# Performance work log

Hardware: AMD Instinct MI355X
Metric: run time of the kernel (lower is better)

## Reference

```python
import jax, jax.numpy as jnp
import numpy as np

B, H, S, D = 65536, 1024, 1024, 128  # batch, hidden_dim, memory_slots, slot_size
WRITE_THRESHOLD = 0.01


def setup_inputs() -> dict:
    key = jax.random.key(0)
    ks = jax.random.split(key, 6)
    return {
        "query": jax.random.normal(ks[0], (B, H), jnp.float32),
        "content": jax.random.normal(ks[1], (B, H), jnp.float32),
        "memory": jax.random.normal(ks[2], (S, D), jnp.float32),
        "memory_age": jnp.zeros((S,), jnp.float32),
        "W_read": jax.random.normal(ks[3], (H, S), jnp.float32) * 0.02,
        "b_read": jnp.zeros((S,), jnp.float32),
        "W_write": jax.random.normal(ks[4], (H, S), jnp.float32) * 0.02,
        "b_write": jnp.zeros((S,), jnp.float32),
        "W_content": jax.random.normal(ks[5], (H, D), jnp.float32) * 0.02,
        "b_content": jnp.zeros((D,), jnp.float32),
    }


def reference(query, content, memory, memory_age, W_read, b_read,
              W_write, b_write, W_content, b_content):
    # ---- read: attention-based addressing over memory slots ----
    read_weights = jax.nn.softmax(query @ W_read + b_read, axis=-1)   # [B, S]
    read_content = read_weights @ memory                              # [B, D]

    # ---- write: vectorized consolidation update (replaces per-slot python loop) ----
    write_weights = jax.nn.softmax(query @ W_write + b_write, axis=-1)  # [B, S]
    w_mean = write_weights.mean(axis=0)                                 # [S]
    c_mean = (content @ W_content + b_content).mean(axis=0)             # [D]
    mask = w_mean > WRITE_THRESHOLD                                     # [S] bool
    consolidation = jax.nn.sigmoid(memory_age * 0.1)                    # [S]
    f = (w_mean * consolidation)[:, None]                               # [S, 1]
    updated = (1.0 - f) * memory + f * c_mean[None, :]                  # [S, D]
    new_memory = jnp.where(mask[:, None], updated, memory)
    new_memory_age = memory_age + mask.astype(memory_age.dtype)

    return read_content, new_memory, new_memory_age
```

## Files before the change

### kernel.cpp

```cpp
#include <hip/hip_runtime.h>
#include <hip/hip_fp16.h>
#include <cstdint>
#include <cstddef>

#define B_N 65536
#define H_N 1024
#define S_N 1024
#define D_N 128

typedef __attribute__((ext_vector_type(8))) short bf16x8;
typedef __attribute__((ext_vector_type(8))) _Float16 f16x8;
typedef __attribute__((ext_vector_type(4))) float f32x4;

#define MFMA_BF(a, b, c) __builtin_amdgcn_mfma_f32_16x16x32_bf16((a), (b), (c), 0, 0, 0)
#define MFMA_F16(a, b, c) __builtin_amdgcn_mfma_f32_16x16x32_f16((a), (b), (c), 0, 0, 0)

__device__ __forceinline__ unsigned short f2bf(float f) {
    unsigned u = __float_as_uint(f);
    u += 0x7FFFu + ((u >> 16) & 1u);
    return (unsigned short)(u >> 16);
}
__device__ __forceinline__ float h2f(unsigned short h) {
    return __half2float(__ushort_as_half(h));
}
__device__ __forceinline__ unsigned short f2h(float f) {
    return __half_as_ushort(__float2half_rn(f));
}
__device__ __forceinline__ void async16(void* lds, const void* g) {
    __builtin_amdgcn_global_load_lds(
        (const __attribute__((address_space(1))) unsigned int*)g,
        (__attribute__((address_space(3))) unsigned int*)lds, 16, 0, 0);
}

__global__ void k_zero(float* p, int n) {
    int i = blockIdx.x * blockDim.x + threadIdx.x;
    if (i < n) p[i] = 0.f;
}

__global__ __launch_bounds__(256) void k_prep_q(const float* __restrict__ q,
                                                unsigned short* __restrict__ qb) {
    size_t i = ((size_t)blockIdx.x * 256 + threadIdx.x) * 8;
    float4 a = *(const float4*)(q + i);
    float4 b = *(const float4*)(q + i + 4);
    uint4 o;
    o.x = (unsigned)f2bf(a.x) | ((unsigned)f2bf(a.y) << 16);
    o.y = (unsigned)f2bf(a.z) | ((unsigned)f2bf(a.w) << 16);
    o.z = (unsigned)f2bf(b.x) | ((unsigned)f2bf(b.y) << 16);
    o.w = (unsigned)f2bf(b.z) | ((unsigned)f2bf(b.w) << 16);
    *(uint4*)(qb + i) = o;
}

__global__ __launch_bounds__(256) void k_prep_w(const float* __restrict__ Wr,
                                                const float* __restrict__ Ww,
                                                unsigned short* __restrict__ wcat) {
    __shared__ float t[32][33];
    const int kb = blockIdx.x * 32, nb = blockIdx.y * 32;
    const float* src = blockIdx.z ? Ww : Wr;
    const int tx = threadIdx.x & 31, ty = threadIdx.x >> 5;
#pragma unroll
    for (int i = 0; i < 4; i++) {
        int r = ty + i * 8;
        t[r][tx] = src[(size_t)(kb + r) * S_N + nb + tx];
    }
    __syncthreads();
    unsigned short* dst = wcat + (size_t)blockIdx.z * 1024 * 1024;
#pragma unroll
    for (int i = 0; i < 4; i++) {
        int r = ty + i * 8;
        dst[(size_t)(nb + r) * 1024 + kb + tx] = f2bf(t[tx][r]);
    }
}

__global__ __launch_bounds__(256) void k_prep_mem(const float* __restrict__ mem,
                                                  unsigned short* __restrict__ memT) {
    __shared__ float t[32][33];
    const int db = blockIdx.x * 32, sb = blockIdx.y * 32;
    const int tx = threadIdx.x & 31, ty = threadIdx.x >> 5;
#pragma unroll
    for (int i = 0; i < 4; i++) {
        int r = ty + i * 8;
        t[r][tx] = mem[(size_t)(sb + r) * D_N + db + tx];
    }
    __syncthreads();
#pragma unroll
    for (int i = 0; i < 4; i++) {
        int r = ty + i * 8;
        memT[(size_t)(db + r) * 1024 + sb + tx] = f2h(t[tx][r]);
    }
}

__global__ __launch_bounds__(256) void k_content(const float* __restrict__ content,
                                                 float* __restrict__ csum) {
    const int tid = threadIdx.x;
    const size_t r0 = (size_t)blockIdx.x * 128;
    float4 a = {0.f, 0.f, 0.f, 0.f};
    const float* base = content + r0 * H_N + tid * 4;
#pragma unroll 8
    for (int r = 0; r < 128; r++) {
        float4 v = *(const float4*)(base + (size_t)r * H_N);
        a.x += v.x; a.y += v.y; a.z += v.z; a.w += v.w;
    }
    atomicAdd(&csum[tid * 4 + 0], a.x);
    atomicAdd(&csum[tid * 4 + 1], a.y);
    atomicAdd(&csum[tid * 4 + 2], a.z);
    atomicAdd(&csum[tid * 4 + 3], a.w);
}

#define BARX() asm volatile("s_barrier" ::: "memory")
#define LGK0() asm volatile("s_waitcnt lgkmcnt(0)" ::: "memory")
#define VMC4() asm volatile("s_waitcnt vmcnt(4)" ::: "memory")

__device__ __forceinline__ bf16x8 ldfrag(const char* buf, int row, int ko) {
    int off = (row * 128 + ko) ^ ((row & 7) << 4);
    return *(const bf16x8*)(buf + off);
}
__device__ __forceinline__ void rd_a(const char* bufA, int wm, int l16, int g, int mh,
                                     bf16x8 a[4][2]) {
#pragma unroll
    for (int m2 = 0; m2 < 4; m2++) {
        int row = wm * 128 + (mh * 4 + m2) * 16 + l16;
#pragma unroll
        for (int ks = 0; ks < 2; ks++) a[m2][ks] = ldfrag(bufA, row, ks * 64 + g * 16);
    }
}
__device__ __forceinline__ void rd_b(const char* bufB, int wn, int l16, int g, int nh,
                                     bf16x8 b[2][2]) {
#pragma unroll
    for (int n2 = 0; n2 < 2; n2++) {
        int row = wn * 64 + (nh * 2 + n2) * 16 + l16;
#pragma unroll
        for (int ks = 0; ks < 2; ks++) b[n2][ks] = ldfrag(bufB, row, ks * 64 + g * 16);
    }
}
__device__ __forceinline__ void mm16(f32x4 acc[8][4], bf16x8 a[4][2], bf16x8 b[2][2],
                                     int mh, int nh) {
    __builtin_amdgcn_s_setprio(1);
#pragma unroll
    for (int m2 = 0; m2 < 4; m2++)
#pragma unroll
        for (int n2 = 0; n2 < 2; n2++) {
            f32x4 c = acc[mh * 4 + m2][nh * 2 + n2];
            c = MFMA_BF(a[m2][0], b[n2][0], c);
            c = MFMA_BF(a[m2][1], b[n2][1], c);
            acc[mh * 4 + m2][nh * 2 + n2] = c;
        }
    __builtin_amdgcn_s_setprio(0);
}

__global__ __launch_bounds__(512, 2) void k_gemm(const unsigned short* __restrict__ qb,
                                                 const unsigned short* __restrict__ wcat,
                                                 const float* __restrict__ b_read,
                                                 const float* __restrict__ b_write,
                                                 unsigned short* __restrict__ logits) {
    __shared__ __align__(16) char sm[131072];
    const int tid = threadIdx.x;
    const int w = tid >> 6, lane = tid & 63;
    const int wm = w >> 2, wn = w & 3;
    const int l16 = lane & 15, g = lane >> 4;

    const int nwg = (int)gridDim.y * 8;
    const int lin = (int)blockIdx.y * 8 + (int)blockIdx.x;
    const int nlin = (lin & 7) * (nwg >> 3) + (lin >> 3);
    const int by = nlin >> 3, bx = nlin & 7;
    const size_t mrow = (size_t)by * 256;

    int g0[2];
#pragma unroll
    for (int j = 0; j < 2; j++) {
        int c = w * 64 + j * 512 + lane;
        int lc = (c * 16) ^ (((c >> 3) & 7) << 4);
        g0[j] = (lc >> 7) * 2048 + (lc & 127);
    }
    const char* aB = (const char*)qb + mrow * 2048;
    const char* wB = (const char*)wcat + (size_t)bx * 256 * 2048;
    char* smW = (char*)sm + w * 1024;

#define STG(d, opb, h, ktB) do {                                              \
        const char* s_ = ((opb) ? wB : aB) + ((h) * 262144 + (ktB));          \
        char* d_ = smW + ((d) * 65536 + (opb) * 32768 + (h) * 16384);         \
        async16(d_,        s_ + g0[0]);                                       \
        async16(d_ + 8192, s_ + g0[1]);                                       \
    } while (0)

    f32x4 acc[8][4];
#pragma unroll
    for (int m = 0; m < 8; m++)
#pragma unroll
        for (int n = 0; n < 4; n++) acc[m][n] = (f32x4){0.f, 0.f, 0.f, 0.f};

    const char* bufA0 = (const char*)sm;
    const char* bufB0 = (const char*)sm + 32768;
    const char* bufA1 = (const char*)sm + 65536;
    const char* bufB1 = (const char*)sm + 98304;
    bf16x8 a[4][2], b0[2][2], b1[2][2];

    STG(0, 0, 0, 0); STG(0, 1, 0, 0); STG(0, 0, 1, 0); STG(0, 1, 1, 0);
    STG(1, 1, 0, 128); STG(1, 1, 1, 128);
    VMC4(); BARX();

#pragma unroll 1
    for (int i = 0; i < 8; i++) {
        const int kA = (2 * i + 1) * 128;
        int t2 = 2 * i + 2; if (t2 > 15) t2 = 15;
        int t3 = 2 * i + 3; if (t3 > 15) t3 = 15;
        const int kB = t2 * 128, kC = t3 * 128;

        rd_a(bufA0, wm, l16, g, 0, a); rd_b(bufB0, wn, l16, g, 0, b0);
        STG(1, 0, 0, kA);
        BARX(); LGK0(); mm16(acc, a, b0, 0, 0); BARX();
        rd_b(bufB0, wn, l16, g, 1, b1);
        STG(1, 0, 1, kA);
        BARX(); LGK0(); mm16(acc, a, b1, 0, 1); BARX();
        rd_a(bufA0, wm, l16, g, 1, a);
        STG(0, 1, 0, kB);
        BARX(); LGK0(); mm16(acc, a, b1, 1, 1); BARX();
        STG(0, 1, 1, kB);
        VMC4(); BARX(); mm16(acc, a, b0, 1, 0); BARX();

        rd_a(bufA1, wm, l16, g, 0, a); rd_b(bufB1, wn, l16, g, 0, b0);
        STG(0, 0, 0, kB);
        BARX(); LGK0(); mm16(acc, a, b0, 0, 0); BARX();
        rd_b(bufB1, wn, l16, g, 1, b1);
        STG(0, 0, 1, kB);
        BARX(); LGK0(); mm16(acc, a, b1, 0, 1); BARX();
        rd_a(bufA1, wm, l16, g, 1, a);
        STG(1, 1, 0, kC);
        BARX(); LGK0(); mm16(acc, a, b1, 1, 1); BARX();
        STG(1, 1, 1, kC);
        VMC4(); BARX(); mm16(acc, a, b0, 1, 0); BARX();
    }
#undef STG

    const float* bias = (bx < 4) ? (b_read + bx * 256) : (b_write + bx * 256 - 1024);
#pragma unroll
    for (int nt = 0; nt < 4; nt++) {
        const int col = wn * 64 + nt * 16 + l16;
        const float bv = bias[col];
#pragma unroll
        for (int mt = 0; mt < 8; mt++) {
            const int row0 = wm * 128 + mt * 16 + g * 4;
#pragma unroll
            for (int r = 0; r < 4; r++) {
                float e = __expf(acc[mt][nt][r] + bv);
                logits[(mrow + row0 + r) * 2048 + (size_t)bx * 256 + col] = f2h(e);
            }
        }
    }
}

__global__ __launch_bounds__(256) void k_post(const unsigned short* __restrict__ logits,
                                              const unsigned short* __restrict__ memT,
                                              float* __restrict__ out,
                                              float* __restrict__ wpart, int blk0) {
    __shared__ unsigned short L[16 * 2056];
    __shared__ float sInvR[16], sInvW[16];
    const int tid = threadIdx.x;
    const size_t r0 = (size_t)blockIdx.x * 16;
#pragma unroll
    for (int i = 0; i < 16; i++) {
        int c2 = i * 256 + tid;
        int r = c2 >> 8, off = (c2 & 255) * 8;
        *(uint4*)&L[r * 2056 + off] = *(const uint4*)&logits[(r0 + r) * 2048 + off];
    }
    __syncthreads();
    {
        const int r = tid >> 4, sub = tid & 15;
        const unsigned* row = (const unsigned*)&L[r * 2056];
        float zr = 0.f, zw = 0.f;
#pragma unroll 8
        for (int i = 0; i < 32; i++) {
            unsigned u = row[i * 16 + sub];
            zr += h2f((unsigned short)(u & 0xffff)) + h2f((unsigned short)(u >> 16));
            unsigned v = row[512 + i * 16 + sub];
            zw += h2f((unsigned short)(v & 0xffff)) + h2f((unsigned short)(v >> 16));
        }
        zr += __shfl_xor(zr, 1); zr += __shfl_xor(zr, 2);
        zr += __shfl_xor(zr, 4); zr += __shfl_xor(zr, 8);
        zw += __shfl_xor(zw, 1); zw += __shfl_xor(zw, 2);
        zw += __shfl_xor(zw, 4); zw += __shfl_xor(zw, 8);
        if (sub == 0) { sInvR[r] = 1.f / zr; sInvW[r] = 1.f / zw; }
    }
    __syncthreads();
    const int wave = tid >> 6, lane = tid & 63;
    const int l16 = lane & 15, g = lane >> 4;
    f32x4 acc0 = (f32x4){0.f, 0.f, 0.f, 0.f}, acc1 = acc0;
    for (int k0 = 0; k0 < 1024; k0 += 32) {
        f16x8 a  = *(const f16x8*)&L[l16 * 2056 + k0 + g * 8];
        f16x8 b0 = *(const f16x8*)&memT[(size_t)(wave * 32 + l16) * 1024 + k0 + g * 8];
        f16x8 b1 = *(const f16x8*)&memT[(size_t)(wave * 32 + 16 + l16) * 1024 + k0 + g * 8];
        acc0 = MFMA_F16(a, b0, acc0);
        acc1 = MFMA_F16(a, b1, acc1);
    }
#pragma unroll
    for (int r = 0; r < 4; r++) {
        int row = g * 4 + r;
        float iz = sInvR[row];
        out[(r0 + row) * D_N + wave * 32 + l16] = acc0[r] * iz;
        out[(r0 + row) * D_N + wave * 32 + 16 + l16] = acc1[r] * iz;
    }
    float c0 = 0.f, c1 = 0.f, c2 = 0.f, c3 = 0.f;
#pragma unroll
    for (int r = 0; r < 16; r++) {
        float iz = sInvW[r];
        uint2 u = *(const uint2*)&L[r * 2056 + 1024 + tid * 4];
        c0 += h2f((unsigned short)(u.x & 0xffff)) * iz;
        c1 += h2f((unsigned short)(u.x >> 16)) * iz;
        c2 += h2f((unsigned short)(u.y & 0xffff)) * iz;
        c3 += h2f((unsigned short)(u.y >> 16)) * iz;
    }
    float4 o = {c0, c1, c2, c3};
    *(float4*)&wpart[(size_t)(blk0 + blockIdx.x) * 1024 + tid * 4] = o;
}

__global__ __launch_bounds__(256) void k_wreduce(const float* __restrict__ wpart,
                                                 float* __restrict__ wsum) {
    const int c = (blockIdx.x & 3) * 256 + threadIdx.x;
    const int i0 = (blockIdx.x >> 2) * 512;
    float s0 = 0.f, s1 = 0.f;
    for (int i = 0; i < 512; i += 2) {
        s0 += wpart[(size_t)(i0 + i) * 1024 + c];
        s1 += wpart[(size_t)(i0 + i + 1) * 1024 + c];
    }
    atomicAdd(&wsum[c], s0 + s1);
}

__global__ void k_cmean(const float* __restrict__ csum, const float* __restrict__ Wc,
                        const float* __restrict__ bc, float* __restrict__ cmean) {
    const int d = blockIdx.x, t = threadIdx.x;
    float s = 0.f;
#pragma unroll
    for (int j = 0; j < 16; j++) {
        int h = j * 64 + t;
        s += csum[h] * Wc[h * D_N + d];
    }
#pragma unroll
    for (int o = 1; o < 64; o <<= 1) s += __shfl_xor(s, o);
    if (t == 0) cmean[d] = s * (1.0f / (float)B_N) + bc[d];
}

__global__ __launch_bounds__(256) void k_final(const float* __restrict__ memory,
                                               const float* __restrict__ age,
                                               const float* __restrict__ wsum,
                                               const float* __restrict__ cmean,
                                               float* __restrict__ out) {
    const int idx = blockIdx.x * 256 + threadIdx.x;
    const int s = idx >> 7, d = idx & 127;
    const float wm = wsum[s] * (1.0f / (float)B_N);
    const bool mask = wm > 0.01f;
    const float cons = 1.0f / (1.0f + __expf(-0.1f * age[s]));
    const float f = wm * cons;
    const float m = memory[idx];
    const float nm = mask ? ((1.0f - f) * m + f * cmean[d]) : m;
    out[(size_t)B_N * D_N + idx] = nm;
    if (d == 0) out[(size_t)B_N * D_N + (size_t)S_N * D_N + s] = age[s] + (mask ? 1.0f : 0.0f);
}

extern "C" void kernel_launch(void* const* d_in, const int* in_sizes, int n_in,
                              void* d_out, int out_size, void* d_ws, size_t ws_size,
                              hipStream_t stream) {
    const float* query    = (const float*)d_in[0];
    const float* content  = (const float*)d_in[1];
    const float* memory   = (const float*)d_in[2];
    const float* age      = (const float*)d_in[3];
    const float* W_read   = (const float*)d_in[4];
    const float* b_read   = (const float*)d_in[5];
    const float* W_write  = (const float*)d_in[6];
    const float* b_write  = (const float*)d_in[7];
    const float* W_cont   = (const float*)d_in[8];
    const float* b_cont   = (const float*)d_in[9];

    char* ws = (char*)d_ws;
    unsigned short* wcat   = (unsigned short*)ws;
    unsigned short* memT   = (unsigned short*)(ws + (4u << 20));
    float* csum            = (float*)(ws + 4456448);
    float* wsum            = csum + 1024;
    float* cmean           = csum + 2048;
    float* wpart           = (float*)(ws + (8u << 20));
    char* dynbase          = ws + (24u << 20);
    float* out = (float*)d_out;

    long long avail = (long long)ws_size - (24ll << 20);
    long long maxrows = avail > 0 ? avail / 6144 : 0;
    int CB = (int)((maxrows / 256) * 256);
    if (CB > B_N) CB = B_N;
    if (CB < 256) CB = 256;
    unsigned short* qbf    = (unsigned short*)dynbase;
    unsigned short* logits = (unsigned short*)(dynbase + (size_t)CB * 2048);

    k_zero<<<8, 256, 0, stream>>>(csum, 2048);
    k_prep_w<<<dim3(32, 32, 2), 256, 0, stream>>>(W_read, W_write, wcat);
    k_prep_mem<<<dim3(4, 32), 256, 0, stream>>>(memory, memT);
    k_content<<<512, 256, 0, stream>>>(content, csum);

    for (int s0 = 0; s0 < B_N; s0 += CB) {
        int rows = B_N - s0;
        if (rows > CB) rows = CB;
        k_prep_q<<<rows / 2, 256, 0, stream>>>(query + (size_t)s0 * H_N, qbf);
        k_gemm<<<dim3(8, rows / 256), 512, 0, stream>>>(qbf, wcat, b_read, b_write, logits);
        k_post<<<rows / 16, 256, 0, stream>>>(logits, memT, out + (size_t)s0 * D_N,
                                              wpart, s0 / 16);
    }
    k_wreduce<<<32, 256, 0, stream>>>(wpart, wsum);
    k_cmean<<<128, 64, 0, stream>>>(csum, W_cont, b_cont, cmean);
    k_final<<<512, 256, 0, stream>>>(memory, age, wsum, cmean, out);
}
```

Measured before the change: 1.114 ms.

## Compute softmax row sums in GEMM epilogue and stage logits through LDS

The GEMM epilogue now computes the exp row sums with shuffles, shared-memory atomics and global atomics into per-row z buffers. It also stages the fp16 logits through swizzled LDS so they are written to global memory as coalesced 8-byte stores. k_post drops its row-sum pass, loads only the read half of the logits into LDS, and reads the write half straight from global memory. The cost is extra global atomics, a zeroing kernel per chunk and one more barrier, and zeroing 131072 floats each chunk assumes the chunk covers all rows.

```diff
diff --git a/kernel.cpp b/kernel.cpp
--- a/kernel.cpp
+++ b/kernel.cpp
@@ -109,6 +109,7 @@
 #define BARX() asm volatile("s_barrier" ::: "memory")
 #define LGK0() asm volatile("s_waitcnt lgkmcnt(0)" ::: "memory")
 #define VMC4() asm volatile("s_waitcnt vmcnt(4)" ::: "memory")
+#define VMC0() asm volatile("s_waitcnt vmcnt(0)" ::: "memory")
 
 __device__ __forceinline__ bf16x8 ldfrag(const char* buf, int row, int ko) {
     int off = (row * 128 + ko) ^ ((row & 7) << 4);
@@ -151,12 +152,17 @@
                                                  const unsigned short* __restrict__ wcat,
                                                  const float* __restrict__ b_read,
                                                  const float* __restrict__ b_write,
-                                                 unsigned short* __restrict__ logits) {
+                                                 unsigned short* __restrict__ logits,
+                                                 float* __restrict__ zr,
+                                                 float* __restrict__ zw) {
     __shared__ __align__(16) char sm[131072];
+    __shared__ float sRow[256];
     const int tid = threadIdx.x;
     const int w = tid >> 6, lane = tid & 63;
     const int wm = w >> 2, wn = w & 3;
     const int l16 = lane & 15, g = lane >> 4;
+
+    if (tid < 256) sRow[tid] = 0.f;
 
     const int nwg = (int)gridDim.y * 8;
     const int lin = (int)blockIdx.y * 8 + (int)blockIdx.x;
@@ -231,61 +237,75 @@
     }
 #undef STG
 
+    VMC0();
+    BARX();
+
     const float* bias = (bx < 4) ? (b_read + bx * 256) : (b_write + bx * 256 - 1024);
-#pragma unroll
-    for (int nt = 0; nt < 4; nt++) {
-        const int col = wn * 64 + nt * 16 + l16;
-        const float bv = bias[col];
-#pragma unroll
-        for (int mt = 0; mt < 8; mt++) {
-            const int row0 = wm * 128 + mt * 16 + g * 4;
-#pragma unroll
-            for (int r = 0; r < 4; r++) {
-                float e = __expf(acc[mt][nt][r] + bv);
-                logits[(mrow + row0 + r) * 2048 + (size_t)bx * 256 + col] = f2h(e);
+    float bcol[4];
+#pragma unroll
+    for (int nt = 0; nt < 4; nt++) bcol[nt] = bias[wn * 64 + nt * 16 + l16];
+
+#pragma unroll
+    for (int mt = 0; mt < 8; mt++) {
+#pragma unroll
+        for (int r = 0; r < 4; r++) {
+            const int row = wm * 128 + mt * 16 + g * 4 + r;
+            const int xr = (row & 15) << 3;
+            float rs = 0.f;
+#pragma unroll
+            for (int nt = 0; nt < 4; nt++) {
+                float e = __expf(acc[mt][nt][r] + bcol[nt]);
+                rs += e;
+                int ofs = ((wn * 64 + nt * 16 + l16) * 2) ^ xr;
+                *(unsigned short*)(sm + row * 512 + ofs) = f2h(e);
             }
+            rs += __shfl_xor(rs, 1); rs += __shfl_xor(rs, 2);
+            rs += __shfl_xor(rs, 4); rs += __shfl_xor(rs, 8);
+            if (l16 == 0) atomicAdd(&sRow[row], rs);
         }
+    }
+    __syncthreads();
+
+    if (tid < 256) {
+        float* zb = (bx < 4) ? zr : zw;
+        atomicAdd(&zb[mrow + tid], sRow[tid]);
+    }
+
+    char* lbase = (char*)logits + mrow * 4096 + (size_t)bx * 512;
+#pragma unroll
+    for (int it = 0; it < 32; it++) {
+        int idx = it * 512 + tid;
+        int row = idx >> 6, sl = idx & 63;
+        int lofs = row * 512 + ((sl * 8) ^ ((row & 15) << 3));
+        uint2 v = *(const uint2*)(sm + lofs);
+        *(uint2*)(lbase + (size_t)row * 4096 + sl * 8) = v;
     }
 }
 
 __global__ __launch_bounds__(256) void k_post(const unsigned short* __restrict__ logits,
                                               const unsigned short* __restrict__ memT,
+                                              const float* __restrict__ zr,
+                                              const float* __restrict__ zw,
                                               float* __restrict__ out,
                                               float* __restrict__ wpart, int blk0) {
-    __shared__ unsigned short L[16 * 2056];
+    __shared__ unsigned short L[16][1032];
     __shared__ float sInvR[16], sInvW[16];
     const int tid = threadIdx.x;
     const size_t r0 = (size_t)blockIdx.x * 16;
 #pragma unroll
-    for (int i = 0; i < 16; i++) {
-        int c2 = i * 256 + tid;
-        int r = c2 >> 8, off = (c2 & 255) * 8;
-        *(uint4*)&L[r * 2056 + off] = *(const uint4*)&logits[(r0 + r) * 2048 + off];
-    }
+    for (int i = 0; i < 8; i++) {
+        int idx = i * 256 + tid;
+        int r = idx >> 7, c = (idx & 127) * 8;
+        *(uint4*)&L[r][c] = *(const uint4*)&logits[(r0 + r) * 2048 + c];
+    }
+    if (tid < 16) { sInvR[tid] = 1.f / zr[r0 + tid]; sInvW[tid] = 1.f / zw[r0 + tid]; }
     __syncthreads();
-    {
-        const int r = tid >> 4, sub = tid & 15;
-        const unsigned* row = (const unsigned*)&L[r * 2056];
-        float zr = 0.f, zw = 0.f;
-#pragma unroll 8
-        for (int i = 0; i < 32; i++) {
-            unsigned u = row[i * 16 + sub];
-            zr += h2f((unsigned short)(u & 0xffff)) + h2f((unsigned short)(u >> 16));
-            unsigned v = row[512 + i * 16 + sub];
-            zw += h2f((unsigned short)(v & 0xffff)) + h2f((unsigned short)(v >> 16));
-        }
-        zr += __shfl_xor(zr, 1); zr += __shfl_xor(zr, 2);
-        zr += __shfl_xor(zr, 4); zr += __shfl_xor(zr, 8);
-        zw += __shfl_xor(zw, 1); zw += __shfl_xor(zw, 2);
-        zw += __shfl_xor(zw, 4); zw += __shfl_xor(zw, 8);
-        if (sub == 0) { sInvR[r] = 1.f / zr; sInvW[r] = 1.f / zw; }
-    }
-    __syncthreads();
+
     const int wave = tid >> 6, lane = tid & 63;
     const int l16 = lane & 15, g = lane >> 4;
     f32x4 acc0 = (f32x4){0.f, 0.f, 0.f, 0.f}, acc1 = acc0;
     for (int k0 = 0; k0 < 1024; k0 += 32) {
-        f16x8 a  = *(const f16x8*)&L[l16 * 2056 + k0 + g * 8];
+        f16x8 a  = *(const f16x8*)&L[l16][k0 + g * 8];
         f16x8 b0 = *(const f16x8*)&memT[(size_t)(wave * 32 + l16) * 1024 + k0 + g * 8];
         f16x8 b1 = *(const f16x8*)&memT[(size_t)(wave * 32 + 16 + l16) * 1024 + k0 + g * 8];
         acc0 = MFMA_F16(a, b0, acc0);
@@ -298,11 +318,12 @@
         out[(r0 + row) * D_N + wave * 32 + l16] = acc0[r] * iz;
         out[(r0 + row) * D_N + wave * 32 + 16 + l16] = acc1[r] * iz;
     }
+
     float c0 = 0.f, c1 = 0.f, c2 = 0.f, c3 = 0.f;
 #pragma unroll
     for (int r = 0; r < 16; r++) {
         float iz = sInvW[r];
-        uint2 u = *(const uint2*)&L[r * 2056 + 1024 + tid * 4];
+        uint2 u = *(const uint2*)&logits[(r0 + r) * 2048 + 1024 + tid * 4];
         c0 += h2f((unsigned short)(u.x & 0xffff)) * iz;
         c1 += h2f((unsigned short)(u.x >> 16)) * iz;
         c2 += h2f((unsigned short)(u.y & 0xffff)) * iz;
@@ -375,6 +396,7 @@
     float* csum            = (float*)(ws + 4456448);
     float* wsum            = csum + 1024;
     float* cmean           = csum + 2048;
+    float* zrow            = (float*)(ws + (5u << 20));
     float* wpart           = (float*)(ws + (8u << 20));
     char* dynbase          = ws + (24u << 20);
     float* out = (float*)d_out;
@@ -395,10 +417,12 @@
     for (int s0 = 0; s0 < B_N; s0 += CB) {
         int rows = B_N - s0;
         if (rows > CB) rows = CB;
+        k_zero<<<512, 256, 0, stream>>>(zrow, 131072);
         k_prep_q<<<rows / 2, 256, 0, stream>>>(query + (size_t)s0 * H_N, qbf);
-        k_gemm<<<dim3(8, rows / 256), 512, 0, stream>>>(qbf, wcat, b_read, b_write, logits);
-        k_post<<<rows / 16, 256, 0, stream>>>(logits, memT, out + (size_t)s0 * D_N,
-                                              wpart, s0 / 16);
+        k_gemm<<<dim3(8, rows / 256), 512, 0, stream>>>(qbf, wcat, b_read, b_write, logits,
+                                                        zrow, zrow + 65536);
+        k_post<<<rows / 16, 256, 0, stream>>>(logits, memT, zrow, zrow + 65536,
+                                              out + (size_t)s0 * D_N, wpart, s0 / 16);
     }
     k_wreduce<<<32, 256, 0, stream>>>(wpart, wsum);
     k_cmean<<<128, 64, 0, stream>>>(csum, W_cont, b_cont, cmean);
```

Result: slower. 1.186 ms (+6.4%).

## Fuse query fp32-to-bf16 conversion into GEMM A-operand loading

Applied to the files above, without the earlier changes.

Removes the separate k_prep_q pass. The GEMM now loads fp32 query tiles into registers, converts them to bf16 with v_cvt_pk_bf16_f32, and writes them swizzled into LDS, while W tiles still stream through async global-to-LDS loads. This drops a full write and re-read of the bf16 query buffer and frees workspace for larger chunks. In exchange, each of the 8 GEMM column blocks re-reads the fp32 query tile at twice the bytes, and the kernel takes on extra VGPR pressure and a more intricate wait and barrier schedule.

```diff
diff --git a/kernel.cpp b/kernel.cpp
--- a/kernel.cpp
+++ b/kernel.cpp
@@ -26,6 +26,11 @@
 __device__ __forceinline__ unsigned short f2h(float f) {
     return __half_as_ushort(__float2half_rn(f));
 }
+__device__ __forceinline__ unsigned cvt2(float lo, float hi) {
+    unsigned d;
+    asm volatile("v_cvt_pk_bf16_f32 %0, %1, %2" : "=v"(d) : "v"(lo), "v"(hi));
+    return d;
+}
 __device__ __forceinline__ void async16(void* lds, const void* g) {
     __builtin_amdgcn_global_load_lds(
         (const __attribute__((address_space(1))) unsigned int*)g,
@@ -35,19 +40,6 @@
 __global__ void k_zero(float* p, int n) {
     int i = blockIdx.x * blockDim.x + threadIdx.x;
     if (i < n) p[i] = 0.f;
-}
-
-__global__ __launch_bounds__(256) void k_prep_q(const float* __restrict__ q,
-                                                unsigned short* __restrict__ qb) {
-    size_t i = ((size_t)blockIdx.x * 256 + threadIdx.x) * 8;
-    float4 a = *(const float4*)(q + i);
-    float4 b = *(const float4*)(q + i + 4);
-    uint4 o;
-    o.x = (unsigned)f2bf(a.x) | ((unsigned)f2bf(a.y) << 16);
-    o.y = (unsigned)f2bf(a.z) | ((unsigned)f2bf(a.w) << 16);
-    o.z = (unsigned)f2bf(b.x) | ((unsigned)f2bf(b.y) << 16);
-    o.w = (unsigned)f2bf(b.z) | ((unsigned)f2bf(b.w) << 16);
-    *(uint4*)(qb + i) = o;
 }
 
 __global__ __launch_bounds__(256) void k_prep_w(const float* __restrict__ Wr,
@@ -108,6 +100,7 @@
 
 #define BARX() asm volatile("s_barrier" ::: "memory")
 #define LGK0() asm volatile("s_waitcnt lgkmcnt(0)" ::: "memory")
+#define VMC8() asm volatile("s_waitcnt vmcnt(8)" ::: "memory")
 #define VMC4() asm volatile("s_waitcnt vmcnt(4)" ::: "memory")
 
 __device__ __forceinline__ bf16x8 ldfrag(const char* buf, int row, int ko) {
@@ -147,7 +140,7 @@
     __builtin_amdgcn_s_setprio(0);
 }
 
-__global__ __launch_bounds__(512, 2) void k_gemm(const unsigned short* __restrict__ qb,
+__global__ __launch_bounds__(512, 2) void k_gemm(const float* __restrict__ qf,
                                                  const unsigned short* __restrict__ wcat,
                                                  const float* __restrict__ b_read,
                                                  const float* __restrict__ b_write,
@@ -171,15 +164,35 @@
         int lc = (c * 16) ^ (((c >> 3) & 7) << 4);
         g0[j] = (lc >> 7) * 2048 + (lc & 127);
     }
-    const char* aB = (const char*)qb + mrow * 2048;
     const char* wB = (const char*)wcat + (size_t)bx * 256 * 2048;
     char* smW = (char*)sm + w * 1024;
 
-#define STG(d, opb, h, ktB) do {                                              \
-        const char* s_ = ((opb) ? wB : aB) + ((h) * 262144 + (ktB));          \
-        char* d_ = smW + ((d) * 65536 + (opb) * 32768 + (h) * 16384);         \
+#define STGB(d, h, ktB) do {                                                  \
+        const char* s_ = wB + ((h) * 262144 + (ktB));                         \
+        char* d_ = smW + ((d) * 65536 + 32768 + (h) * 16384);                 \
         async16(d_,        s_ + g0[0]);                                       \
         async16(d_ + 8192, s_ + g0[1]);                                       \
+    } while (0)
+
+    const int arow = tid >> 2;
+    const float* aF = qf + (mrow + arow) * 1024 + (tid & 3) * 16;
+    float4 av0[4], av1[4];
+#define ALD(dst, h, kt) do {                                                  \
+        const float* s_ = aF + (h) * 131072 + (kt) * 64;                      \
+        dst[0] = *(const float4*)(s_);      dst[1] = *(const float4*)(s_ + 4);\
+        dst[2] = *(const float4*)(s_ + 8);  dst[3] = *(const float4*)(s_ + 12);\
+    } while (0)
+#define AWR(d, h, fv) do {                                                    \
+        char* base_ = (char*)sm + (d) * 65536 + (h) * 16384;                  \
+        const int lb0_ = (tid & 3) * 32;                                      \
+        const int xr_ = (arow & 7) << 4;                                      \
+        uint4 p0_, p1_;                                                       \
+        p0_.x = cvt2(fv[0].x, fv[0].y); p0_.y = cvt2(fv[0].z, fv[0].w);       \
+        p0_.z = cvt2(fv[1].x, fv[1].y); p0_.w = cvt2(fv[1].z, fv[1].w);       \
+        p1_.x = cvt2(fv[2].x, fv[2].y); p1_.y = cvt2(fv[2].z, fv[2].w);       \
+        p1_.z = cvt2(fv[3].x, fv[3].y); p1_.w = cvt2(fv[3].z, fv[3].w);       \
+        *(uint4*)(base_ + ((arow * 128 + lb0_) ^ xr_)) = p0_;                 \
+        *(uint4*)(base_ + ((arow * 128 + lb0_ + 16) ^ xr_)) = p1_;            \
     } while (0)
 
     f32x4 acc[8][4];
@@ -194,42 +207,53 @@
     const char* bufB1 = (const char*)sm + 98304;
     bf16x8 a[4][2], b0[2][2], b1[2][2];
 
-    STG(0, 0, 0, 0); STG(0, 1, 0, 0); STG(0, 0, 1, 0); STG(0, 1, 1, 0);
-    STG(1, 1, 0, 128); STG(1, 1, 1, 128);
-    VMC4(); BARX();
+    ALD(av0, 0, 0); ALD(av1, 1, 0);
+    STGB(0, 0, 0); STGB(0, 1, 0);
+    STGB(1, 0, 128); STGB(1, 1, 128);
+    VMC8();
+    AWR(0, 0, av0); AWR(0, 1, av1);
+    VMC4();
+    LGK0();
+    BARX();
 
 #pragma unroll 1
     for (int i = 0; i < 8; i++) {
-        const int kA = (2 * i + 1) * 128;
+        const int tA = 2 * i + 1;
         int t2 = 2 * i + 2; if (t2 > 15) t2 = 15;
         int t3 = 2 * i + 3; if (t3 > 15) t3 = 15;
         const int kB = t2 * 128, kC = t3 * 128;
 
         rd_a(bufA0, wm, l16, g, 0, a); rd_b(bufB0, wn, l16, g, 0, b0);
-        STG(1, 0, 0, kA);
+        ALD(av0, 0, tA);
         BARX(); LGK0(); mm16(acc, a, b0, 0, 0); BARX();
         rd_b(bufB0, wn, l16, g, 1, b1);
-        STG(1, 0, 1, kA);
+        ALD(av1, 1, tA);
         BARX(); LGK0(); mm16(acc, a, b1, 0, 1); BARX();
         rd_a(bufA0, wm, l16, g, 1, a);
-        STG(0, 1, 0, kB);
+        STGB(0, 0, kB);
         BARX(); LGK0(); mm16(acc, a, b1, 1, 1); BARX();
-        STG(0, 1, 1, kB);
-        VMC4(); BARX(); mm16(acc, a, b0, 1, 0); BARX();
+        STGB(0, 1, kB);
+        VMC4();
+        AWR(1, 0, av0); AWR(1, 1, av1);
+        LGK0(); BARX(); mm16(acc, a, b0, 1, 0); BARX();
 
         rd_a(bufA1, wm, l16, g, 0, a); rd_b(bufB1, wn, l16, g, 0, b0);
-        STG(0, 0, 0, kB);
+        ALD(av0, 0, t2);
         BARX(); LGK0(); mm16(acc, a, b0, 0, 0); BARX();
         rd_b(bufB1, wn, l16, g, 1, b1);
-        STG(0, 0, 1, kB);
+        ALD(av1, 1, t2);
         BARX(); LGK0(); mm16(acc, a, b1, 0, 1); BARX();
         rd_a(bufA1, wm, l16, g, 1, a);
-        STG(1, 1, 0, kC);
+        STGB(1, 0, kC);
         BARX(); LGK0(); mm16(acc, a, b1, 1, 1); BARX();
-        STG(1, 1, 1, kC);
-        VMC4(); BARX(); mm16(acc, a, b0, 1, 0); BARX();
-    }
-#undef STG
+        STGB(1, 1, kC);
+        VMC4();
+        AWR(0, 0, av0); AWR(0, 1, av1);
+        LGK0(); BARX(); mm16(acc, a, b0, 1, 0); BARX();
+    }
+#undef STGB
+#undef ALD
+#undef AWR
 
     const float* bias = (bx < 4) ? (b_read + bx * 256) : (b_write + bx * 256 - 1024);
 #pragma unroll
@@ -380,12 +404,11 @@
     float* out = (float*)d_out;
 
     long long avail = (long long)ws_size - (24ll << 20);
-    long long maxrows = avail > 0 ? avail / 6144 : 0;
+    long long maxrows = avail > 0 ? avail / 4096 : 0;
     int CB = (int)((maxrows / 256) * 256);
     if (CB > B_N) CB = B_N;
     if (CB < 256) CB = 256;
-    unsigned short* qbf    = (unsigned short*)dynbase;
-    unsigned short* logits = (unsigned short*)(dynbase + (size_t)CB * 2048);
+    unsigned short* logits = (unsigned short*)dynbase;
 
     k_zero<<<8, 256, 0, stream>>>(csum, 2048);
     k_prep_w<<<dim3(32, 32, 2), 256, 0, stream>>>(W_read, W_write, wcat);
@@ -395,8 +418,8 @@
     for (int s0 = 0; s0 < B_N; s0 += CB) {
         int rows = B_N - s0;
         if (rows > CB) rows = CB;
-        k_prep_q<<<rows / 2, 256, 0, stream>>>(query + (size_t)s0 * H_N, qbf);
-        k_gemm<<<dim3(8, rows / 256), 512, 0, stream>>>(qbf, wcat, b_read, b_write, logits);
+        k_gemm<<<dim3(8, rows / 256), 512, 0, stream>>>(query + (size_t)s0 * H_N, wcat,
+                                                        b_read, b_write, logits);
         k_post<<<rows / 16, 256, 0, stream>>>(logits, memT, out + (size_t)s0 * D_N,
                                               wpart, s0 / 16);
     }
```

Measured after the change: 1.392 ms. 1.25x slower.
